# Performance work log

Hardware: AMD Instinct MI355X
Metric: run time of the kernel (lower is better)

Reference implementation:

```python
import jax, jax.numpy as jnp
import numpy as np

HEAD_DIM = 64  # hidden_dim 1024 // heads_num 16


def setup_inputs() -> dict:
    key = jax.random.key(0)
    ks = jax.random.split(key, 5)
    B, S, H = 2, 4096, 1024
    std = 1.0 / np.sqrt(H)
    return {
        "x": jax.random.normal(ks[0], (B, S, H), jnp.float32),
        "Wq": jax.random.normal(ks[1], (H, H), jnp.float32) * std,
        "bq": jnp.zeros((H,), jnp.float32),
        "Wk": jax.random.normal(ks[2], (H, H), jnp.float32) * std,
        "bk": jnp.zeros((H,), jnp.float32),
        "Wv": jax.random.normal(ks[3], (H, H), jnp.float32) * std,
        "bv": jnp.zeros((H,), jnp.float32),
        "Wo": jax.random.normal(ks[4], (H, H), jnp.float32) * std,
        "bo": jnp.zeros((H,), jnp.float32),
    }


def reference(x, Wq, bq, Wk, bk, Wv, bv, Wo, bo):
    # Linear projections (torch Linear: x @ W^T + b)
    q = jnp.einsum("bsh,oh->bso", x, Wq) + bq
    k = jnp.einsum("bsh,oh->bso", x, Wk) + bk
    v = jnp.einsum("bsh,oh->bso", x, Wv) + bv
    # all_to_all is identity on a single device (world size 1)
    scale = jnp.float32(HEAD_DIM) ** 0.5
    # Faithful to source: attention over the FULL hidden dim (no head split),
    # full [B, S, S] score matrix.
    scores = jnp.einsum("bqh,bkh->bqk", q, k) / scale
    weights = jax.nn.softmax(scores, axis=-1)
    attn = jnp.einsum("bqk,bkh->bqh", weights, v)
    out = jnp.einsum("bsh,oh->bso", attn, Wo) + bo
    return out
```

## Files before the change

### kernel.cpp

```cpp
#include <hip/hip_runtime.h>
#include <stdint.h>


typedef __bf16 bf16x8 __attribute__((ext_vector_type(8)));
typedef float  f32x4  __attribute__((ext_vector_type(4)));

__device__ __forceinline__ unsigned short f32_to_bf16_rne(float f) {
    uint32_t u = __builtin_bit_cast(uint32_t, f);
    uint32_t r = (u + 0x7FFFu + ((u >> 16) & 1u)) >> 16;
    return (unsigned short)r;
}

#define BM 128
#define BN 128
#define BK 64

__global__ __launch_bounds__(256) void cvt_all(
    const float* __restrict__ x,
    const float* __restrict__ Wq, const float* __restrict__ Wk,
    const float* __restrict__ Wo, const float* __restrict__ Wv,
    const float* __restrict__ bq,
    const float* __restrict__ bv, const float* __restrict__ bo,
    unsigned short* __restrict__ x16, unsigned short* __restrict__ w16,
    float* __restrict__ rsum, float* __restrict__ bfinal,
    float* __restrict__ g0)
{
    const int b = blockIdx.x, tid = threadIdx.x;
    if (b < 8192) {
        int i = (b * 256 + tid) * 4;
        float4 v = *(const float4*)(x + i);
        ushort4 o;
        o.x = f32_to_bf16_rne(v.x); o.y = f32_to_bf16_rne(v.y);
        o.z = f32_to_bf16_rne(v.z); o.w = f32_to_bf16_rne(v.w);
        *(ushort4*)(x16 + i) = o;
    } else if (b < 9216) {
        int i = ((b - 8192) * 256 + tid) * 4;
        float4 v = *(const float4*)(Wo + i);
        ushort4 o;
        o.x = f32_to_bf16_rne(v.x); o.y = f32_to_bf16_rne(v.y);
        o.z = f32_to_bf16_rne(v.z); o.w = f32_to_bf16_rne(v.w);
        *(ushort4*)(w16 + (size_t)2 * 1048576 + i) = o;
    } else if (b < 9984) {
        __shared__ unsigned short tl[64 * 68];
        int t = b - 9216;
        int which = t >> 8;
        const float* src = which == 0 ? Wq : which == 1 ? Wk : Wv;
        size_t slot = which == 0 ? 0 : which == 1 ? 1 : 3;
        int tile = t & 255, tr = tile >> 4, tc = tile & 15;
        #pragma unroll
        for (int it = 0; it < 4; ++it) {
            int r  = it * 16 + (tid >> 4);
            int c0 = (tid & 15) * 4;
            float4 v = *(const float4*)(src + (size_t)(tr * 64 + r) * 1024 + tc * 64 + c0);
            tl[(c0 + 0) * 68 + r] = f32_to_bf16_rne(v.x);
            tl[(c0 + 1) * 68 + r] = f32_to_bf16_rne(v.y);
            tl[(c0 + 2) * 68 + r] = f32_to_bf16_rne(v.z);
            tl[(c0 + 3) * 68 + r] = f32_to_bf16_rne(v.w);
        }
        __syncthreads();
        #pragma unroll
        for (int it = 0; it < 4; ++it) {
            int c  = it * 16 + (tid >> 4);
            int r0 = (tid & 15) * 4;
            ushort4 o;
            o.x = tl[c * 68 + r0 + 0]; o.y = tl[c * 68 + r0 + 1];
            o.z = tl[c * 68 + r0 + 2]; o.w = tl[c * 68 + r0 + 3];
            *(ushort4*)(w16 + slot * 1048576 + (size_t)(tc * 64 + c) * 1024 + tr * 64 + r0) = o;
        }
    } else if (b < 10000) {
        int bb = b - 9984;
        int lane = tid & 63, wv_ = tid >> 6;
        int rowBase = bb * 64 + wv_ * 16;
        for (int rr = 0; rr < 16; ++rr) {
            int row = rowBase + rr;
            float partial = 0.f;
            #pragma unroll
            for (int t2 = 0; t2 < 16; ++t2) {
                int h = t2 * 64 + lane;
                partial += Wo[(size_t)row * 1024 + h] * bv[h];
            }
            #pragma unroll
            for (int off = 32; off > 0; off >>= 1)
                partial += __shfl_xor(partial, off, 64);
            if (lane == 0) bfinal[row] = bo[row] + partial;
        }
    } else if (b < 10004) {
        int j = (b - 10000) * 256 + tid;
        float acc = 0.f;
        #pragma unroll 8
        for (int h = 0; h < 1024; ++h) acc += bq[h] * Wk[(size_t)h * 1024 + j];
        g0[j] = acc;
    } else {
        int i = (b - 10004) * 1024 + tid * 4;
        *(float4*)(rsum + i) = float4{0.f, 0.f, 0.f, 0.f};
    }
}

__device__ __forceinline__ void gemm_core(
    const unsigned short* __restrict__ Ab,
    const unsigned short* __restrict__ Bb,
    unsigned short* ldsA, unsigned short* ldsB,
    int mBase, int nBase, int lane, int wave, int K, f32x4 (&acc)[4][4])
{
    const int quad = lane >> 4;
    const int l16  = lane & 15;
    const int wr   = wave >> 1;
    const int wc   = wave & 1;

    for (int k0 = 0; k0 < K; k0 += BK) {
        #pragma unroll
        for (int i = 0; i < 4; ++i) {
            int base = (i * 4 + wave) * 64;
            int s    = base + lane;
            int row  = s >> 3;
            int col  = ((s ^ (s >> 3)) & 7) * 8;
            __builtin_amdgcn_global_load_lds(
                (const __attribute__((address_space(1))) void*)(Ab + (size_t)(mBase + row) * K + (size_t)(k0 + col)),
                (__attribute__((address_space(3))) void*)(&ldsA[base * 8]),
                16, 0, 0);
        }
        #pragma unroll
        for (int i = 0; i < 4; ++i) {
            int base = (i * 4 + wave) * 64;
            int s    = base + lane;
            int row  = s >> 3;
            int col  = ((s ^ (s >> 3)) & 7) * 8;
            __builtin_amdgcn_global_load_lds(
                (const __attribute__((address_space(1))) void*)(Bb + (size_t)(nBase + row) * K + (size_t)(k0 + col)),
                (__attribute__((address_space(3))) void*)(&ldsB[base * 8]),
                16, 0, 0);
        }
        __syncthreads();

        #pragma unroll
        for (int kk = 0; kk < 2; ++kk) {
            bf16x8 af[4], bfv[4];
            #pragma unroll
            for (int mi = 0; mi < 4; ++mi) {
                int r = wr * 64 + mi * 16 + l16;
                int c = kk * 4 + quad;
                af[mi] = *(const bf16x8*)(&ldsA[r * BK + (((c ^ r) & 7) << 3)]);
            }
            #pragma unroll
            for (int ni = 0; ni < 4; ++ni) {
                int r = wc * 64 + ni * 16 + l16;
                int c = kk * 4 + quad;
                bfv[ni] = *(const bf16x8*)(&ldsB[r * BK + (((c ^ r) & 7) << 3)]);
            }
            #pragma unroll
            for (int mi = 0; mi < 4; ++mi)
                #pragma unroll
                for (int ni = 0; ni < 4; ++ni)
                    acc[mi][ni] = __builtin_amdgcn_mfma_f32_16x16x32_bf16(
                        af[mi], bfv[ni], acc[mi][ni], 0, 0, 0);
        }
        __syncthreads();
    }
}

__global__ __launch_bounds__(256) void gemm_gf(
    const unsigned short* __restrict__ w16,
    unsigned short* __restrict__ Gt16, unsigned short* __restrict__ F16)
{
    __shared__ unsigned short ldsA[BM * BK];
    __shared__ unsigned short ldsB[BN * BK];

    const int l = blockIdx.x, tid = threadIdx.x;
    const unsigned short *Ab, *Bb;
    unsigned short* Cb;
    int f;
    if (l < 64) { f = l;      Ab = w16 + (size_t)1 * 1048576; Bb = w16;                        Cb = Gt16; }
    else        { f = l - 64; Ab = w16 + (size_t)2 * 1048576; Bb = w16 + (size_t)3 * 1048576; Cb = F16;  }
    int mBase = (f >> 3) * BM, nBase = (f & 7) * BN;

    const int lane = tid & 63, wave = tid >> 6;
    const int quad = lane >> 4, l16 = lane & 15;
    const int wr = wave >> 1, wc = wave & 1;

    f32x4 acc[4][4] = {};
    gemm_core(Ab, Bb, ldsA, ldsB, mBase, nBase, lane, wave, 1024, acc);

    #pragma unroll
    for (int mi = 0; mi < 4; ++mi)
        #pragma unroll
        for (int ni = 0; ni < 4; ++ni) {
            int col = nBase + wc * 64 + ni * 16 + l16;
            #pragma unroll
            for (int r = 0; r < 4; ++r) {
                int row = mBase + wr * 64 + mi * 16 + quad * 4 + r;
                Cb[(size_t)row * 1024 + col] = f32_to_bf16_rne(acc[mi][ni][r]);
            }
        }
}

__global__ __launch_bounds__(256) void gemm_qgv(
    const unsigned short* __restrict__ x16,
    const unsigned short* __restrict__ Gt16,
    const unsigned short* __restrict__ F16,
    const float* __restrict__ g0,
    unsigned short* __restrict__ qg16,
    unsigned short* __restrict__ vot16)
{
    __shared__ unsigned short ldsA[BM * BK];
    __shared__ unsigned short ldsB[BN * BK];

    int l   = blockIdx.x;
    int idx = (l & 7) * 128 + (l >> 3);

    const unsigned short *Ab, *Bb;
    unsigned short* Cb;
    const float* bias;
    int mBase, nBase, Cstride;
    if (idx < 512) {
        mBase = (idx >> 3) * BM; nBase = (idx & 7) * BN;
        Ab = x16; Bb = Gt16; Cb = qg16; bias = g0; Cstride = 1024;
    } else {
        int v = idx - 512;
        int zb = v >> 8, t2 = v & 255;
        mBase = (t2 >> 5) * BM; nBase = (t2 & 31) * BN;
        Ab = F16; Bb = x16 + (size_t)zb * 4096 * 1024;
        Cb = vot16 + (size_t)zb * 1024 * 4096; bias = nullptr; Cstride = 4096;
    }

    const int tid  = threadIdx.x;
    const int lane = tid & 63;
    const int wave = tid >> 6;
    const int quad = lane >> 4;
    const int l16  = lane & 15;
    const int wr   = wave >> 1;
    const int wc   = wave & 1;

    f32x4 acc[4][4] = {};
    gemm_core(Ab, Bb, ldsA, ldsB, mBase, nBase, lane, wave, 1024, acc);

    #pragma unroll
    for (int mi = 0; mi < 4; ++mi)
        #pragma unroll
        for (int ni = 0; ni < 4; ++ni) {
            int col = nBase + wc * 64 + ni * 16 + l16;
            float b = bias ? bias[col] : 0.f;
            #pragma unroll
            for (int r = 0; r < 4; ++r) {
                int row = mBase + wr * 64 + mi * 16 + quad * 4 + r;
                Cb[(size_t)row * Cstride + col] = f32_to_bf16_rne(acc[mi][ni][r] + b);
            }
        }
}

template <int MODE>
__global__ __launch_bounds__(256) void gemm_bt(
    const unsigned short* __restrict__ A,
    const unsigned short* __restrict__ Bt,
    void* __restrict__ C,
    const float* __restrict__ b0, float* __restrict__ rowsum,
    float alpha, int M, int N, int K,
    long long aZ, long long bZ, long long cZ)
{
    __shared__ unsigned short ldsA[BM * BK];
    __shared__ unsigned short ldsB[BN * BK];

    const int NB = gridDim.x, MBt = gridDim.y;
    int l  = blockIdx.x + gridDim.x * (blockIdx.y + gridDim.y * blockIdx.z);
    int xcd = l & 7;
    int t   = l >> 3;
    int MBX = MBt >> 1;
    int NBX = NB >> 2;
    int mbl = t % MBX;
    int r1  = t / MBX;
    int nbi = r1 % NBX;
    int zb  = r1 / NBX;
    int mb  = (xcd >> 2) * MBX + mbl;
    int nb  = (xcd & 3) * NBX + nbi;

    const unsigned short* Ab = A  + (size_t)zb * aZ;
    const unsigned short* Bb = Bt + (size_t)zb * bZ;

    const int tid  = threadIdx.x;
    const int lane = tid & 63;
    const int wave = tid >> 6;
    const int quad = lane >> 4;
    const int l16  = lane & 15;
    const int wr   = wave >> 1;
    const int wc   = wave & 1;
    const int mBase = mb * BM;
    const int nBase = nb * BN;

    f32x4 acc[4][4] = {};
    gemm_core(Ab, Bb, ldsA, ldsB, mBase, nBase, lane, wave, K, acc);

    if (MODE == 3) {
        unsigned short* Pz = (unsigned short*)C + (size_t)zb * cZ;
        float* rs = rowsum + (size_t)zb * M;
        #pragma unroll
        for (int mi = 0; mi < 4; ++mi) {
            #pragma unroll
            for (int r = 0; r < 4; ++r) {
                int row = mBase + wr * 64 + mi * 16 + quad * 4 + r;
                float e[4];
                float partial = 0.f;
                #pragma unroll
                for (int ni = 0; ni < 4; ++ni) {
                    e[ni] = __expf(acc[mi][ni][r] * alpha);
                    partial += e[ni];
                }
                #pragma unroll
                for (int ni = 0; ni < 4; ++ni) {
                    int col = nBase + wc * 64 + ni * 16 + l16;
                    Pz[(size_t)row * N + col] = f32_to_bf16_rne(e[ni]);
                }
                #pragma unroll
                for (int off = 1; off < 16; off <<= 1)
                    partial += __shfl_xor(partial, off, 64);
                if (l16 == 0) atomicAdd(&rs[row], partial);
            }
        }
    }
}

template <int MODE, int BMt, int BNt>
__global__ __launch_bounds__(512) void gemm8p(
    const unsigned short* __restrict__ A,
    const unsigned short* __restrict__ Bt,
    void* __restrict__ C,
    const float* __restrict__ b0, float* __restrict__ rowsum,
    float alpha, int M, int N, int K,
    long long aZ, long long bZ, long long cZ,
    int MBt, int NB)
{
    constexpr int RW  = BMt / 2;
    constexpr int CW  = BNt / 4;
    constexpr int MI  = RW / 16;
    constexpr int NI  = CW / 16;
    constexpr int NPH = MI / 2;
    constexpr int BL  = (BNt * 64 / 512) / 8;
    constexpr int NWT = BL + NPH - 1;

    __shared__ __align__(16) unsigned short ldsA[2][BMt * 64];
    __shared__ __align__(16) unsigned short ldsB[2][BNt * 64];

    const int l   = blockIdx.x;
    const int xcd = l & 7;
    const int t   = l >> 3;
    const int MBX = MBt >> 1;
    const int NBX = NB >> 2;
    const int mbl = t % MBX;
    const int r1  = t / MBX;
    const int nbi = r1 % NBX;
    const int zb  = r1 / NBX;
    const int mb  = (xcd >> 2) * MBX + mbl;
    const int nb  = (xcd & 3) * NBX + nbi;

    const unsigned short* Ab = A  + (size_t)zb * aZ;
    const unsigned short* Bb = Bt + (size_t)zb * bZ;

    const int tid  = threadIdx.x;
    const int lane = tid & 63;
    const int wave = tid >> 6;
    const int quad = lane >> 4;
    const int l16  = lane & 15;
    const int wr   = wave >> 2;
    const int wc   = wave & 3;
    const int mBase = mb * BMt;
    const int nBase = nb * BNt;
    const int NT    = K >> 6;

    const int aRow0 = ((wave & 4) ? RW : 0) + (wave & 3) * 8;

    auto stageA = [&](int p, int kt, int q) {
        const int rowbase = aRow0 + q * 32;
        const int row = rowbase + (lane >> 3);
        const int col = (((lane & 7) ^ row) & 7) << 3;
        __builtin_amdgcn_global_load_lds(
            (const __attribute__((address_space(1))) void*)(
                Ab + (size_t)(mBase + row) * K + (size_t)((kt << 6) + col)),
            (__attribute__((address_space(3))) void*)(&ldsA[p][rowbase * 64]),
            16, 0, 0);
    };
    auto stageB = [&](int p, int kt) {
        #pragma unroll
        for (int i = 0; i < BL; ++i) {
            const int g   = wave * BL + i;
            const int row = (g << 3) + (lane >> 3);
            const int col = (((lane & 7) ^ row) & 7) << 3;
            __builtin_amdgcn_global_load_lds(
                (const __attribute__((address_space(1))) void*)(
                    Bb + (size_t)(nBase + row) * K + (size_t)((kt << 6) + col)),
                (__attribute__((address_space(3))) void*)(&ldsB[p][g << 9]),
                16, 0, 0);
        }
    };

    bf16x8 bf[NI][2];
    bf16x8 af[2][2];
    auto ldB = [&](int p) {
        #pragma unroll
        for (int n2 = 0; n2 < NI; ++n2)
            #pragma unroll
            for (int kk = 0; kk < 2; ++kk) {
                const int r = wc * CW + n2 * 16 + l16;
                const int c = kk * 4 + quad;
                bf[n2][kk] = *(const bf16x8*)&ldsB[p][r * 64 + (((c ^ r) & 7) << 3)];
            }
    };
    auto ldA = [&](int p, int q) {
        #pragma unroll
        for (int m2 = 0; m2 < 2; ++m2)
            #pragma unroll
            for (int kk = 0; kk < 2; ++kk) {
                const int r = wr * RW + (q * 2 + m2) * 16 + l16;
                const int c = kk * 4 + quad;
                af[m2][kk] = *(const bf16x8*)&ldsA[p][r * 64 + (((c ^ r) & 7) << 3)];
            }
    };

    f32x4 acc[MI][NI] = {};

    stageB(0, 0);
    #pragma unroll
    for (int q = 0; q < NPH; ++q) stageA(0, 0, q);
    if (NT > 1) {
        stageB(1, 1);
        #pragma unroll
        for (int q = 0; q < NPH - 1; ++q) stageA(1, 1, q);
        asm volatile("s_waitcnt vmcnt(%0)" :: "n"(NWT) : "memory");
    } else {
        asm volatile("s_waitcnt vmcnt(0)" ::: "memory");
    }
    __builtin_amdgcn_s_barrier();

    for (int kt = 0; kt < NT; ++kt) {
        const int p = kt & 1;
        #pragma unroll
        for (int q = 0; q < NPH; ++q) {
            if (q == 0) ldB(p);
            ldA(p, q);
            if (q == 0) {
                if (kt + 1 < NT) stageA(p ^ 1, kt + 1, NPH - 1);
            } else if (q == 1) {
                if (kt + 2 < NT) { stageB(p, kt + 2); stageA(p, kt + 2, 0); }
            } else {
                if (kt + 2 < NT) stageA(p, kt + 2, q - 1);
            }
            if (q == NPH - 1) {
                if (kt + 2 < NT) {
                    asm volatile("s_waitcnt vmcnt(%0)" :: "n"(NWT) : "memory");
                } else if (kt + 1 < NT) {
                    asm volatile("s_waitcnt vmcnt(0)" ::: "memory");
                }
            }
            __builtin_amdgcn_s_barrier();
            asm volatile("s_waitcnt lgkmcnt(0)" ::: "memory");
            __builtin_amdgcn_sched_barrier(0);
            __builtin_amdgcn_s_setprio(1);
            #pragma unroll
            for (int m2 = 0; m2 < 2; ++m2)
                #pragma unroll
                for (int n2 = 0; n2 < NI; ++n2)
                    #pragma unroll
                    for (int kk = 0; kk < 2; ++kk)
                        acc[q * 2 + m2][n2] = __builtin_amdgcn_mfma_f32_16x16x32_bf16(
                            af[m2][kk], bf[n2][kk], acc[q * 2 + m2][n2], 0, 0, 0);
            __builtin_amdgcn_s_setprio(0);
            __builtin_amdgcn_s_barrier();
        }
    }

    {
        float* Cz = (float*)C + (size_t)zb * cZ;
        const float* rs = rowsum + (size_t)zb * M;
        #pragma unroll
        for (int mi = 0; mi < MI; ++mi) {
            #pragma unroll
            for (int r = 0; r < 4; ++r) {
                const int row = mBase + wr * RW + mi * 16 + quad * 4 + r;
                const float inv = 1.f / rs[row];
                #pragma unroll
                for (int ni = 0; ni < NI; ++ni) {
                    const int col = nBase + wc * CW + ni * 16 + l16;
                    Cz[(size_t)row * N + col] = acc[mi][ni][r] * inv + b0[col];
                }
            }
        }
    }
}

extern "C" void kernel_launch(void* const* d_in, const int* in_sizes, int n_in,
                              void* d_out, int out_size, void* d_ws, size_t ws_size,
                              hipStream_t stream)
{
    const float* x  = (const float*)d_in[0];
    const float* Wq = (const float*)d_in[1];
    const float* bq = (const float*)d_in[2];
    const float* Wk = (const float*)d_in[3];
    const float* bv = (const float*)d_in[6];
    const float* Wv = (const float*)d_in[5];
    const float* Wo = (const float*)d_in[7];
    const float* bo = (const float*)d_in[8];
    float* out = (float*)d_out;

    const int S = 4096, H = 1024, Bsz = 2;
    const int M = Bsz * S;

    char* p = (char*)d_ws;
    auto alloc = [&](size_t bytes) -> char* {
        char* r = p; p += (bytes + 255) & ~(size_t)255; return r;
    };
    unsigned short* w16   = (unsigned short*)alloc((size_t)4 * H * H * 2);
    unsigned short* F16   = (unsigned short*)alloc((size_t)H * H * 2);
    unsigned short* Gt16  = (unsigned short*)alloc((size_t)H * H * 2);
    unsigned short* qg16  = (unsigned short*)alloc((size_t)M * H * 2);
    unsigned short* vot16 = (unsigned short*)alloc((size_t)Bsz * H * S * 2);
    unsigned short* x16   = (unsigned short*)alloc((size_t)M * H * 2);
    float*          rsum  = (float*)alloc((size_t)M * 4);
    float*          bfin  = (float*)alloc((size_t)H * 4);
    float*          g0    = (float*)alloc((size_t)H * 4);
    unsigned short* p16   = (unsigned short*)alloc((size_t)Bsz * S * S * 2);

    cvt_all<<<10012, 256, 0, stream>>>(x, Wq, Wk, Wo, Wv, bq, bv, bo,
                                       x16, w16, rsum, bfin, g0);

    gemm_gf<<<128, 256, 0, stream>>>(w16, Gt16, F16);

    gemm_qgv<<<1024, 256, 0, stream>>>(x16, Gt16, F16, g0, qg16, vot16);

    gemm_bt<3><<<dim3(S / BN, S / BM, 2), 256, 0, stream>>>(
        qg16, x16, p16, nullptr, rsum, 0.125f, S, S, 1024,
        (long long)S * H, (long long)S * H, (long long)S * S);

    gemm8p<6, 128, 256><<<256, 512, 0, stream>>>(
        p16, vot16, out, bfin, rsum, 1.f, S, H, 4096,
        (long long)S * S, (long long)H * S, (long long)S * H, 32, 4);
}
```

Before: 378.1 us.

## Move score/exp GEMM onto 8-wave pipelined kernel with 256x256 tiles

The QK^T score GEMM with fused exp and row-sum now runs on the 512-thread pipelined gemm8p kernel with 256x256 tiles, replacing the 256-thread 128x128 gemm_bt kernel. The aim is more data reuse per tile and better MFMA pipelining on the largest GEMM. The bq·Wk bias-vector reduction is split over 64 blocks using float4 loads and atomicAdd, instead of 4 serial 1024-iteration loops. rsum and g0 are now zeroed with hipMemsetAsync, which adds small launches and makes the g0 sum order nondeterministic.

Measured after the change: 349.2 us. 7.6% less time.

```diff
diff --git a/kernel.cpp b/kernel.cpp
--- a/kernel.cpp
+++ b/kernel.cpp
@@ -22,8 +22,7 @@
     const float* __restrict__ bq,
     const float* __restrict__ bv, const float* __restrict__ bo,
     unsigned short* __restrict__ x16, unsigned short* __restrict__ w16,
-    float* __restrict__ rsum, float* __restrict__ bfinal,
-    float* __restrict__ g0)
+    float* __restrict__ bfinal, float* __restrict__ g0)
 {
     const int b = blockIdx.x, tid = threadIdx.x;
     if (b < 8192) {
@@ -84,15 +83,19 @@
                 partial += __shfl_xor(partial, off, 64);
             if (lane == 0) bfinal[row] = bo[row] + partial;
         }
-    } else if (b < 10004) {
-        int j = (b - 10000) * 256 + tid;
-        float acc = 0.f;
-        #pragma unroll 8
-        for (int h = 0; h < 1024; ++h) acc += bq[h] * Wk[(size_t)h * 1024 + j];
-        g0[j] = acc;
     } else {
-        int i = (b - 10004) * 1024 + tid * 4;
-        *(float4*)(rsum + i) = float4{0.f, 0.f, 0.f, 0.f};
+        int bb = b - 10000;
+        int j0 = tid * 4;
+        float ax = 0.f, ay = 0.f, az = 0.f, aw = 0.f;
+        #pragma unroll
+        for (int r = 0; r < 16; ++r) {
+            int h = bb * 16 + r;
+            float s = bq[h];
+            float4 w = *(const float4*)(Wk + (size_t)h * 1024 + j0);
+            ax += s * w.x; ay += s * w.y; az += s * w.z; aw += s * w.w;
+        }
+        atomicAdd(&g0[j0 + 0], ax); atomicAdd(&g0[j0 + 1], ay);
+        atomicAdd(&g0[j0 + 2], az); atomicAdd(&g0[j0 + 3], aw);
     }
 }
 
@@ -247,76 +250,6 @@
         }
 }
 
-template <int MODE>
-__global__ __launch_bounds__(256) void gemm_bt(
-    const unsigned short* __restrict__ A,
-    const unsigned short* __restrict__ Bt,
-    void* __restrict__ C,
-    const float* __restrict__ b0, float* __restrict__ rowsum,
-    float alpha, int M, int N, int K,
-    long long aZ, long long bZ, long long cZ)
-{
-    __shared__ unsigned short ldsA[BM * BK];
-    __shared__ unsigned short ldsB[BN * BK];
-
-    const int NB = gridDim.x, MBt = gridDim.y;
-    int l  = blockIdx.x + gridDim.x * (blockIdx.y + gridDim.y * blockIdx.z);
-    int xcd = l & 7;
-    int t   = l >> 3;
-    int MBX = MBt >> 1;
-    int NBX = NB >> 2;
-    int mbl = t % MBX;
-    int r1  = t / MBX;
-    int nbi = r1 % NBX;
-    int zb  = r1 / NBX;
-    int mb  = (xcd >> 2) * MBX + mbl;
-    int nb  = (xcd & 3) * NBX + nbi;
-
-    const unsigned short* Ab = A  + (size_t)zb * aZ;
-    const unsigned short* Bb = Bt + (size_t)zb * bZ;
-
-    const int tid  = threadIdx.x;
-    const int lane = tid & 63;
-    const int wave = tid >> 6;
-    const int quad = lane >> 4;
-    const int l16  = lane & 15;
-    const int wr   = wave >> 1;
-    const int wc   = wave & 1;
-    const int mBase = mb * BM;
-    const int nBase = nb * BN;
-
-    f32x4 acc[4][4] = {};
-    gemm_core(Ab, Bb, ldsA, ldsB, mBase, nBase, lane, wave, K, acc);
-
-    if (MODE == 3) {
-        unsigned short* Pz = (unsigned short*)C + (size_t)zb * cZ;
-        float* rs = rowsum + (size_t)zb * M;
-        #pragma unroll
-        for (int mi = 0; mi < 4; ++mi) {
-            #pragma unroll
-            for (int r = 0; r < 4; ++r) {
-                int row = mBase + wr * 64 + mi * 16 + quad * 4 + r;
-                float e[4];
-                float partial = 0.f;
-                #pragma unroll
-                for (int ni = 0; ni < 4; ++ni) {
-                    e[ni] = __expf(acc[mi][ni][r] * alpha);
-                    partial += e[ni];
-                }
-                #pragma unroll
-                for (int ni = 0; ni < 4; ++ni) {
-                    int col = nBase + wc * 64 + ni * 16 + l16;
-                    Pz[(size_t)row * N + col] = f32_to_bf16_rne(e[ni]);
-                }
-                #pragma unroll
-                for (int off = 1; off < 16; off <<= 1)
-                    partial += __shfl_xor(partial, off, 64);
-                if (l16 == 0) atomicAdd(&rs[row], partial);
-            }
-        }
-    }
-}
-
 template <int MODE, int BMt, int BNt>
 __global__ __launch_bounds__(512) void gemm8p(
     const unsigned short* __restrict__ A,
@@ -465,7 +398,33 @@
         }
     }
 
-    {
+    if constexpr (MODE == 3) {
+        unsigned short* Pz = (unsigned short*)C + (size_t)zb * cZ;
+        float* rs = rowsum + (size_t)zb * M;
+        #pragma unroll
+        for (int mi = 0; mi < MI; ++mi) {
+            #pragma unroll
+            for (int r = 0; r < 4; ++r) {
+                const int row = mBase + wr * RW + mi * 16 + quad * 4 + r;
+                float e[NI];
+                float partial = 0.f;
+                #pragma unroll
+                for (int ni = 0; ni < NI; ++ni) {
+                    e[ni] = __expf(acc[mi][ni][r] * alpha);
+                    partial += e[ni];
+                }
+                #pragma unroll
+                for (int ni = 0; ni < NI; ++ni) {
+                    const int col = nBase + wc * CW + ni * 16 + l16;
+                    Pz[(size_t)row * N + col] = f32_to_bf16_rne(e[ni]);
+                }
+                #pragma unroll
+                for (int off = 1; off < 16; off <<= 1)
+                    partial += __shfl_xor(partial, off, 64);
+                if (l16 == 0) atomicAdd(&rs[row], partial);
+            }
+        }
+    } else {
         float* Cz = (float*)C + (size_t)zb * cZ;
         const float* rs = rowsum + (size_t)zb * M;
         #pragma unroll
@@ -492,8 +451,8 @@
     const float* Wq = (const float*)d_in[1];
     const float* bq = (const float*)d_in[2];
     const float* Wk = (const float*)d_in[3];
+    const float* Wv = (const float*)d_in[5];
     const float* bv = (const float*)d_in[6];
-    const float* Wv = (const float*)d_in[5];
     const float* Wo = (const float*)d_in[7];
     const float* bo = (const float*)d_in[8];
     float* out = (float*)d_out;
@@ -516,16 +475,19 @@
     float*          g0    = (float*)alloc((size_t)H * 4);
     unsigned short* p16   = (unsigned short*)alloc((size_t)Bsz * S * S * 2);
 
-    cvt_all<<<10012, 256, 0, stream>>>(x, Wq, Wk, Wo, Wv, bq, bv, bo,
-                                       x16, w16, rsum, bfin, g0);
+    hipMemsetAsync(rsum, 0, (size_t)M * 4, stream);
+    hipMemsetAsync(g0,   0, (size_t)H * 4, stream);
+
+    cvt_all<<<10064, 256, 0, stream>>>(x, Wq, Wk, Wo, Wv, bq, bv, bo,
+                                       x16, w16, bfin, g0);
 
     gemm_gf<<<128, 256, 0, stream>>>(w16, Gt16, F16);
 
     gemm_qgv<<<1024, 256, 0, stream>>>(x16, Gt16, F16, g0, qg16, vot16);
 
-    gemm_bt<3><<<dim3(S / BN, S / BM, 2), 256, 0, stream>>>(
+    gemm8p<3, 256, 256><<<512, 512, 0, stream>>>(
         qg16, x16, p16, nullptr, rsum, 0.125f, S, S, 1024,
-        (long long)S * H, (long long)S * H, (long long)S * S);
+        (long long)S * H, (long long)S * H, (long long)S * S, 16, 16);
 
     gemm8p<6, 128, 256><<<256, 512, 0, stream>>>(
         p16, vot16, out, bfin, rsum, 1.f, S, H, 4096,
```
